# Performance work log

Hardware: AMD Instinct MI355X
Metric: run time of the kernel (lower is better)

Reference implementation:

```python
import jax, jax.numpy as jnp
import numpy as np
from functools import partial

EPS = 1e-6

def rmsnorm(x, w):
    rms = jnp.sqrt(jnp.mean(x * x, axis=-1, keepdims=True) + EPS)
    return x * w / rms

def causal_dwconv(x, w):
    # x: [B, T, D], w: [D, 1, k] depthwise kernel (torch Conv1d layout)
    D = x.shape[-1]
    k = w.shape[-1]
    xt = jnp.transpose(x, (0, 2, 1))  # [B, D, T]
    out = jax.lax.conv_general_dilated(
        xt, w, window_strides=(1,), padding=[(k - 1, 0)],
        dimension_numbers=("NCH", "OIH", "NCH"), feature_group_count=D)
    return jnp.transpose(out, (0, 2, 1))  # [B, T, D]

def setup_inputs() -> dict:
    key = jax.random.key(0)
    B, T, D, F, S = 2, 4096, 1024, 4096, 4096
    ks = jax.random.split(key, 20)
    s = 0.02
    return {
        "x": jax.random.normal(ks[0], (B, T, D), jnp.float32),
        "h_prev": jnp.zeros((B, D), jnp.float32),
        "norm1_w": jnp.ones((D,), jnp.float32),
        "conv3_w": jax.random.normal(ks[1], (D, 1, 3), jnp.float32) * s,
        "conv7_w": jax.random.normal(ks[2], (D, 1, 7), jnp.float32) * s,
        "conv15_w": jax.random.normal(ks[3], (D, 1, 15), jnp.float32) * s,
        "mix_w": jax.random.normal(ks[4], (D, D), jnp.float32) * s,
        "norm2_w": jnp.ones((D,), jnp.float32),
        "Wz_w": jax.random.normal(ks[5], (D, D), jnp.float32) * s,
        "Wz_b": jnp.zeros((D,), jnp.float32),
        "Wh_w": jax.random.normal(ks[6], (D, D), jnp.float32) * s,
        "Wh_b": jnp.zeros((D,), jnp.float32),
        "norm3_w": jnp.ones((D,), jnp.float32),
        "slot_keys": jax.random.normal(ks[7], (S, D), jnp.float32) * s,
        "slot_values": jax.random.normal(ks[8], (S, D), jnp.float32) * s,
        "projq_w": jax.random.normal(ks[9], (D, D), jnp.float32) * s,
        "projout_w": jax.random.normal(ks[10], (D, D), jnp.float32) * s,
        "norm4_w": jnp.ones((D,), jnp.float32),
        "gate_w": jax.random.normal(ks[11], (F, D), jnp.float32) * s,
        "up_w": jax.random.normal(ks[12], (F, D), jnp.float32) * s,
        "down_w": jax.random.normal(ks[13], (D, F), jnp.float32) * s,
    }

def resonance_forward(x, h_prev, norm1_w, conv3_w, conv7_w, conv15_w, mix_w,
                      norm2_w, Wz_w, Wz_b, Wh_w, Wh_b, norm3_w, slot_keys,
                      slot_values, projq_w, projout_w, norm4_w, gate_w, up_w, down_w):
    B, T, D = x.shape
    top_k = 2
    # 1. multi-scale causal conv block
    xn = rmsnorm(x, norm1_w)
    conv = causal_dwconv(xn, conv3_w) + causal_dwconv(xn, conv7_w) + causal_dwconv(xn, conv15_w)
    x = x + conv @ mix_w.T
    # 2. MinGRU: precompute gates, then linear recurrence via scan
    xn = rmsnorm(x, norm2_w)
    z = jax.nn.sigmoid(xn @ Wz_w.T + Wz_b)        # [B, T, D]
    h_tilde = xn @ Wh_w.T + Wh_b                  # [B, T, D]
    def step(h, zh):
        zt, ht = zh
        h = (1.0 - zt) * h + zt * ht
        return h, h
    h_last, hs = jax.lax.scan(step, h_prev,
                              (jnp.swapaxes(z, 0, 1), jnp.swapaxes(h_tilde, 0, 1)))
    x = x + jnp.swapaxes(hs, 0, 1)
    # 3. slot memory with top-k routing
    xn = rmsnorm(x, norm3_w)
    q = xn @ projq_w.T
    scores = (q @ slot_keys.T) / jnp.sqrt(jnp.asarray(D, x.dtype))  # [B, T, S]
    topk_vals, topk_ids = jax.lax.top_k(scores, top_k)              # [B, T, k]
    attn = jax.nn.softmax(topk_vals, axis=-1)
    gathered = slot_values[topk_ids]                                # [B, T, k, D]
    retrieved = jnp.einsum("btk,btkd->btd", attn, gathered)
    x = x + retrieved @ projout_w.T
    # 4. SwiGLU FFN
    xn = rmsnorm(x, norm4_w)
    ff = (jax.nn.silu(xn @ gate_w.T) * (xn @ up_w.T)) @ down_w.T
    x = x + ff
    return x, h_last

def reference(x, h_prev, norm1_w, conv3_w, conv7_w, conv15_w, mix_w, norm2_w,
              Wz_w, Wz_b, Wh_w, Wh_b, norm3_w, slot_keys, slot_values,
              projq_w, projout_w, norm4_w, gate_w, up_w, down_w):
    return resonance_forward(x, h_prev, norm1_w, conv3_w, conv7_w, conv15_w,
                             mix_w, norm2_w, Wz_w, Wz_b, Wh_w, Wh_b, norm3_w,
                             slot_keys, slot_values, projq_w, projout_w,
                             norm4_w, gate_w, up_w, down_w)
```

## Files before the change

### kernel.cpp

```cpp
#include <hip/hip_runtime.h>
#include <hip/hip_bf16.h>
#include <cstdint>

#define BB   2
#define TT   4096
#define DD   1024
#define FF   4096
#define SS   4096
#define MTOK (BB * TT)
#define NCHUNK 32
#define TCHUNK 128

typedef __bf16 bf16x8 __attribute__((ext_vector_type(8)));
typedef float  f32x4  __attribute__((ext_vector_type(4)));
typedef __attribute__((address_space(3))) char lds_char;
typedef __attribute__((address_space(1))) char g_char;

struct CvtArgs {
  const float* src[9];
  __hip_bfloat16* dst[9];
  int off4[10];
};

__global__ __launch_bounds__(256) void cvt_all_kernel(CvtArgs a) {
  int g = blockIdx.x * 256 + threadIdx.x;
  if (g >= a.off4[9]) return;
  int s = 0;
  while (g >= a.off4[s + 1]) s++;
  int i = g - a.off4[s];
  float4 v = ((const float4*)a.src[s])[i];
  union { ushort4 u; __hip_bfloat16 h[4]; } p;
  p.h[0] = __float2bfloat16(v.x);
  p.h[1] = __float2bfloat16(v.y);
  p.h[2] = __float2bfloat16(v.z);
  p.h[3] = __float2bfloat16(v.w);
  ((ushort4*)a.dst[s])[i] = p.u;
}

__global__ void wcomb_kernel(const float* __restrict__ w3, const float* __restrict__ w7,
                             const float* __restrict__ w15, float* __restrict__ wc) {
  int d = blockIdx.x * 256 + threadIdx.x;
  if (d >= DD) return;
  for (int j = 0; j < 16; j++) {
    float v = 0.f;
    if (j < 15) {
      v = w15[d * 15 + (14 - j)];
      if (j < 7) v += w7[d * 7 + (6 - j)];
      if (j < 3) v += w3[d * 3 + (2 - j)];
    }
    wc[d * 16 + j] = v;
  }
}

__global__ __launch_bounds__(256) void rms_kernel(const float* __restrict__ x,
                                                  const float* __restrict__ w,
                                                  __hip_bfloat16* __restrict__ ob) {
  const int row = blockIdx.x;
  const int tid = threadIdx.x;
  float4 v = ((const float4*)(x + (size_t)row * DD))[tid];
  float ss = v.x * v.x + v.y * v.y + v.z * v.z + v.w * v.w;
  for (int off = 32; off > 0; off >>= 1) ss += __shfl_down(ss, off, 64);
  __shared__ float wsum[4];
  if ((tid & 63) == 0) wsum[tid >> 6] = ss;
  __syncthreads();
  float tot = wsum[0] + wsum[1] + wsum[2] + wsum[3];
  float rinv = 1.0f / sqrtf(tot * (1.0f / DD) + 1e-6f);
  float4 wg = ((const float4*)w)[tid];
  union { ushort4 u; __hip_bfloat16 h[4]; } p;
  p.h[0] = __float2bfloat16(v.x * wg.x * rinv);
  p.h[1] = __float2bfloat16(v.y * wg.y * rinv);
  p.h[2] = __float2bfloat16(v.z * wg.z * rinv);
  p.h[3] = __float2bfloat16(v.w * wg.w * rinv);
  ((ushort4*)ob)[(size_t)row * 256 + tid] = p.u;
}

__global__ __launch_bounds__(256) void conv_kernel(const __hip_bfloat16* __restrict__ xn,
                                                   const float* __restrict__ wc,
                                                   __hip_bfloat16* __restrict__ outp) {
  __shared__ float xt[78][64];
  __shared__ float wt[64][15];
  const int b = blockIdx.z, t0 = blockIdx.x * 64, d0 = blockIdx.y * 64;
  const int tid = threadIdx.x;
  const int dl = tid & 63;
  for (int idx = tid; idx < 64 * 15; idx += 256) {
    int d = idx / 15, j = idx % 15;
    wt[d][j] = wc[(d0 + d) * 16 + j];
  }
  for (int r = tid >> 6; r < 78; r += 4) {
    int t = t0 - 14 + r;
    xt[r][dl] = (t >= 0) ? __bfloat162float(xn[((size_t)b * TT + t) * DD + d0 + dl]) : 0.f;
  }
  __syncthreads();
  for (int tl = tid >> 6; tl < 64; tl += 4) {
    float acc = 0.f;
#pragma unroll
    for (int j = 0; j < 15; j++) acc += wt[dl][j] * xt[tl + 14 - j][dl];
    outp[((size_t)b * TT + t0 + tl) * DD + d0 + dl] = __float2bfloat16(acc);
  }
}

template <int EPI>
__global__ __launch_bounds__(256, 2) void gemm_bt(
    const __hip_bfloat16* __restrict__ A, const __hip_bfloat16* __restrict__ Bm,
    const int M, const int N, const int K,
    const float* __restrict__ resid, float* __restrict__ outf,
    __hip_bfloat16* __restrict__ outb,
    const float* __restrict__ bias0, const float* __restrict__ bias1,
    const __hip_bfloat16* __restrict__ mulin) {
  __shared__ __align__(16) __hip_bfloat16 As[128 * 32];
  __shared__ __align__(16) __hip_bfloat16 Bs[128 * 32];
  const int tid = threadIdx.x;
  const int lane = tid & 63;
  const int wave = tid >> 6;
  const int fm = lane & 15, fq = lane >> 4;

  const int nT = gridDim.x;
  const int lin = blockIdx.y * nT + blockIdx.x;
  const int xcd = lin & 7;
  const int idx_ = lin >> 3;
  const int mq = idx_ / nT;
  const int tileM = (xcd * (gridDim.y >> 3) + mq) * 128;
  const int tileN = (idx_ - mq * nT) * 128;

  const int wm = (wave & 1) * 64, wn = (wave >> 1) * 64;

  f32x4 acc[4][4] = {};

  const int srow = tid >> 2;
  const int scol = (tid & 3) * 8;
  const __hip_bfloat16* gA = A + (size_t)(tileM + srow) * K + scol;
  const __hip_bfloat16* gB = Bm + (size_t)(tileN + srow) * K + scol;
  lds_char* ldsA = (lds_char*)(&As[0]);
  lds_char* ldsB = (lds_char*)(&Bs[0]);
  const int wbyte = wave * 1024;

  for (int k0 = 0; k0 < K; k0 += 32) {
    __syncthreads();
    __builtin_amdgcn_global_load_lds((g_char*)(void*)(gA + k0),                  ldsA + wbyte,        16, 0, 0);
    __builtin_amdgcn_global_load_lds((g_char*)(void*)(gA + k0 + (size_t)64 * K), ldsA + wbyte + 4096, 16, 0, 0);
    __builtin_amdgcn_global_load_lds((g_char*)(void*)(gB + k0),                  ldsB + wbyte,        16, 0, 0);
    __builtin_amdgcn_global_load_lds((g_char*)(void*)(gB + k0 + (size_t)64 * K), ldsB + wbyte + 4096, 16, 0, 0);
    __syncthreads();
    bf16x8 af[4], bfr[4];
#pragma unroll
    for (int i = 0; i < 4; i++) {
      af[i]  = *(const bf16x8*)(As + (wm + i * 16 + fm) * 32 + fq * 8);
      bfr[i] = *(const bf16x8*)(Bs + (wn + i * 16 + fm) * 32 + fq * 8);
    }
#pragma unroll
    for (int i = 0; i < 4; i++)
#pragma unroll
      for (int j = 0; j < 4; j++)
        acc[i][j] = __builtin_amdgcn_mfma_f32_16x16x32_bf16(af[i], bfr[j], acc[i][j], 0, 0, 0);
  }

#pragma unroll
  for (int i = 0; i < 4; i++) {
#pragma unroll
    for (int j = 0; j < 4; j++) {
      const int c = tileN + wn + j * 16 + fm;
#pragma unroll
      for (int r = 0; r < 4; r++) {
        const int rw = tileM + wm + i * 16 + fq * 4 + r;
        const size_t idx = (size_t)rw * N + c;
        float v = acc[i][j][r];
        if constexpr (EPI == 0) {
          outf[idx] = resid[idx] + v;
        } else if constexpr (EPI == 1) {
          v += (c < DD) ? bias0[c] : bias1[c - DD];
          if (c < DD) v = 1.f / (1.f + __expf(-v));
          outb[idx] = __float2bfloat16(v);
        } else if constexpr (EPI == 2) {
          outb[idx] = __float2bfloat16(v);
        } else if constexpr (EPI == 4) {
          outb[idx] = __float2bfloat16(v / (1.f + __expf(-v)));
        } else {
          outb[idx] = __float2bfloat16(v * __bfloat162float(mulin[idx]));
        }
      }
    }
  }
}

__global__ __launch_bounds__(256) void scan_pass1(const __hip_bfloat16* __restrict__ zht,
                                                  float* __restrict__ cA,
                                                  float* __restrict__ cB) {
  const int b = blockIdx.z, c = blockIdx.y;
  const int d = blockIdx.x * 256 + threadIdx.x;
  const __hip_bfloat16* base = zht + (size_t)b * TT * 2048;
  float A = 1.f, Bc = 0.f;
  const int t0 = c * TCHUNK;
  for (int t = t0; t < t0 + TCHUNK; t++) {
    const __hip_bfloat16* rowp = base + (size_t)t * 2048;
    float z = __bfloat162float(rowp[d]);
    float h = __bfloat162float(rowp[DD + d]);
    float om = 1.f - z;
    A *= om;
    Bc = om * Bc + z * h;
  }
  size_t idx = ((size_t)b * NCHUNK + c) * DD + d;
  cA[idx] = A;
  cB[idx] = Bc;
}

__global__ __launch_bounds__(256) void scan_pass2(const float* __restrict__ hp,
                                                  const float* __restrict__ cA,
                                                  const float* __restrict__ cB,
                                                  float* __restrict__ hstart,
                                                  float* __restrict__ hlast) {
  const int b = blockIdx.y;
  const int d = blockIdx.x * 256 + threadIdx.x;
  float h = hp[b * DD + d];
  for (int c = 0; c < NCHUNK; c++) {
    size_t idx = ((size_t)b * NCHUNK + c) * DD + d;
    hstart[idx] = h;
    h = cA[idx] * h + cB[idx];
  }
  hlast[b * DD + d] = h;
}

__global__ __launch_bounds__(256) void scan_pass3(const __hip_bfloat16* __restrict__ zht,
                                                  const float* __restrict__ hstart,
                                                  float* __restrict__ x) {
  const int b = blockIdx.z, c = blockIdx.y;
  const int d = blockIdx.x * 256 + threadIdx.x;
  const __hip_bfloat16* base = zht + (size_t)b * TT * 2048;
  float h = hstart[((size_t)b * NCHUNK + c) * DD + d];
  const int t0 = c * TCHUNK;
  for (int t = t0; t < t0 + TCHUNK; t++) {
    const __hip_bfloat16* rowp = base + (size_t)t * 2048;
    float z = __bfloat162float(rowp[d]);
    float ht = __bfloat162float(rowp[DD + d]);
    h = (1.f - z) * h + z * ht;
    x[((size_t)b * TT + t) * DD + d] += h;
  }
}

__global__ __launch_bounds__(256) void topk_kernel(const __hip_bfloat16* __restrict__ scores,
                                                   const float* __restrict__ sv,
                                                   __hip_bfloat16* __restrict__ ret) {
  const int row = blockIdx.x;
  const int tid = threadIdx.x;
  const __hip_bfloat16* sr = scores + (size_t)row * SS;
  float v0 = -3.4e38f, v1 = -3.4e38f;
  int i0 = 0x7fffffff, i1 = 0x7fffffff;
#pragma unroll
  for (int it = 0; it < 2; it++) {
    int j0 = (it * 256 + tid) * 8;
    bf16x8 v8 = *(const bf16x8*)(sr + j0);
#pragma unroll
    for (int k = 0; k < 8; k++) {
      float v = (float)v8[k];
      int j = j0 + k;
      if (v > v0) { v1 = v0; i1 = i0; v0 = v; i0 = j; }
      else if (v > v1) { v1 = v; i1 = j; }
    }
  }
#define TKMERGE(w0, j0, w1, j1)                                              \
  {                                                                          \
    if (w0 > v0 || (w0 == v0 && j0 < i0)) {                                  \
      float t0v = v0; int t0i = i0; v0 = w0; i0 = j0;                        \
      if (t0v > w1 || (t0v == w1 && t0i < j1)) { v1 = t0v; i1 = t0i; }       \
      else { v1 = w1; i1 = j1; }                                             \
    } else {                                                                 \
      if (w0 > v1 || (w0 == v1 && j0 < i1)) { v1 = w0; i1 = j0; }            \
    }                                                                        \
  }
  for (int off = 32; off > 0; off >>= 1) {
    float w0 = __shfl_down(v0, off, 64), w1 = __shfl_down(v1, off, 64);
    int   j0 = __shfl_down(i0, off, 64), j1 = __shfl_down(i1, off, 64);
    TKMERGE(w0, j0, w1, j1);
  }
  __shared__ float wv0[4], wv1[4];
  __shared__ int   wi0[4], wi1[4];
  __shared__ float sattn[2];
  __shared__ int   sidx[2];
  if ((tid & 63) == 0) { int w = tid >> 6; wv0[w] = v0; wv1[w] = v1; wi0[w] = i0; wi1[w] = i1; }
  __syncthreads();
  if (tid == 0) {
    v0 = wv0[0]; i0 = wi0[0]; v1 = wv1[0]; i1 = wi1[0];
    for (int w = 1; w < 4; w++) { TKMERGE(wv0[w], wi0[w], wv1[w], wi1[w]); }
    float s0 = v0 * (1.f / 32.f), s1 = v1 * (1.f / 32.f);
    float e = __expf(s1 - s0);
    float denom = 1.f + e;
    sattn[0] = 1.f / denom;
    sattn[1] = e / denom;
    sidx[0] = i0; sidx[1] = i1;
  }
  __syncthreads();
  float a0 = sattn[0], a1 = sattn[1];
  const float4* r0 = (const float4*)(sv + (size_t)sidx[0] * DD);
  const float4* r1 = (const float4*)(sv + (size_t)sidx[1] * DD);
  float4 u = r0[tid], w4 = r1[tid];
  union { ushort4 u; __hip_bfloat16 h[4]; } p;
  p.h[0] = __float2bfloat16(a0 * u.x + a1 * w4.x);
  p.h[1] = __float2bfloat16(a0 * u.y + a1 * w4.y);
  p.h[2] = __float2bfloat16(a0 * u.z + a1 * w4.z);
  p.h[3] = __float2bfloat16(a0 * u.w + a1 * w4.w);
  ((ushort4*)(ret + (size_t)row * DD))[tid] = p.u;
#undef TKMERGE
}

extern "C" void kernel_launch(void* const* d_in, const int* in_sizes, int n_in,
                              void* d_out, int out_size, void* d_ws, size_t ws_size,
                              hipStream_t stream) {
  (void)in_sizes; (void)n_in; (void)out_size; (void)ws_size;
  const float* x_in   = (const float*)d_in[0];
  const float* h_prev = (const float*)d_in[1];
  const float* n1w    = (const float*)d_in[2];
  const float* w3     = (const float*)d_in[3];
  const float* w7     = (const float*)d_in[4];
  const float* w15    = (const float*)d_in[5];
  const float* mixw   = (const float*)d_in[6];
  const float* n2w    = (const float*)d_in[7];
  const float* wzw    = (const float*)d_in[8];
  const float* wzb    = (const float*)d_in[9];
  const float* whw    = (const float*)d_in[10];
  const float* whb    = (const float*)d_in[11];
  const float* n3w    = (const float*)d_in[12];
  const float* slotk  = (const float*)d_in[13];
  const float* slotv  = (const float*)d_in[14];
  const float* pqw    = (const float*)d_in[15];
  const float* pow_   = (const float*)d_in[16];
  const float* n4w    = (const float*)d_in[17];
  const float* gatew  = (const float*)d_in[18];
  const float* upw    = (const float*)d_in[19];
  const float* downw  = (const float*)d_in[20];
  float* out = (float*)d_out;

  char* ws = (char*)d_ws;
  size_t o = 0;
  auto alloc = [&](size_t bytes) {
    size_t r = o;
    o += (bytes + 255) & ~(size_t)255;
    return r;
  };
  __hip_bfloat16* wmix = (__hip_bfloat16*)(ws + alloc((size_t)DD * DD * 2));
  __hip_bfloat16* wzht = (__hip_bfloat16*)(ws + alloc((size_t)2 * DD * DD * 2));
  __hip_bfloat16* wpq  = (__hip_bfloat16*)(ws + alloc((size_t)DD * DD * 2));
  __hip_bfloat16* wsk  = (__hip_bfloat16*)(ws + alloc((size_t)SS * DD * 2));
  __hip_bfloat16* wpo  = (__hip_bfloat16*)(ws + alloc((size_t)DD * DD * 2));
  __hip_bfloat16* wg   = (__hip_bfloat16*)(ws + alloc((size_t)FF * DD * 2));
  __hip_bfloat16* wu   = (__hip_bfloat16*)(ws + alloc((size_t)FF * DD * 2));
  __hip_bfloat16* wd   = (__hip_bfloat16*)(ws + alloc((size_t)DD * FF * 2));
  float* wcomb = (float*)(ws + alloc((size_t)DD * 16 * 4));
  float* xws   = (float*)(ws + alloc((size_t)MTOK * DD * 4));
  __hip_bfloat16* xnb  = (__hip_bfloat16*)(ws + alloc((size_t)MTOK * DD * 2));
  __hip_bfloat16* qb   = (__hip_bfloat16*)(ws + alloc((size_t)MTOK * DD * 2));
  __hip_bfloat16* retr = (__hip_bfloat16*)(ws + alloc((size_t)MTOK * DD * 2));
  float* scanA  = (float*)(ws + alloc((size_t)BB * NCHUNK * DD * 4));
  float* scanB  = (float*)(ws + alloc((size_t)BB * NCHUNK * DD * 4));
  float* hstart = (float*)(ws + alloc((size_t)BB * NCHUNK * DD * 4));
  char* big = ws + alloc((size_t)MTOK * FF * 4);
  __hip_bfloat16* xn1b  = (__hip_bfloat16*)big;
  __hip_bfloat16* convb = (__hip_bfloat16*)(big + (size_t)MTOK * DD * 2);
  __hip_bfloat16* zhtb  = (__hip_bfloat16*)big;
  __hip_bfloat16* scoresb = (__hip_bfloat16*)big;
  __hip_bfloat16* sg    = (__hip_bfloat16*)big;
  __hip_bfloat16* ffin  = (__hip_bfloat16*)(big + (size_t)MTOK * FF * 2);

  {
    CvtArgs a;
    const float* srcs[9] = {mixw, wzw, whw, pqw, slotk, pow_, gatew, upw, downw};
    __hip_bfloat16* dsts[9] = {wmix, wzht, wzht + (size_t)DD * DD, wpq, wsk, wpo, wg, wu, wd};
    int n4s[9] = {DD * DD / 4, DD * DD / 4, DD * DD / 4, DD * DD / 4, SS * DD / 4,
                  DD * DD / 4, FF * DD / 4, FF * DD / 4, DD * FF / 4};
    int acc_ = 0;
    for (int i = 0; i < 9; i++) { a.src[i] = srcs[i]; a.dst[i] = dsts[i]; a.off4[i] = acc_; acc_ += n4s[i]; }
    a.off4[9] = acc_;
    cvt_all_kernel<<<(acc_ + 255) / 256, 256, 0, stream>>>(a);
  }
  wcomb_kernel<<<DD / 256, 256, 0, stream>>>(w3, w7, w15, wcomb);

  rms_kernel<<<MTOK, 256, 0, stream>>>(x_in, n1w, xn1b);
  conv_kernel<<<dim3(TT / 64, DD / 64, BB), 256, 0, stream>>>(xn1b, wcomb, convb);
  gemm_bt<0><<<dim3(DD / 128, MTOK / 128), 256, 0, stream>>>(
      convb, wmix, MTOK, DD, DD, x_in, xws, nullptr, nullptr, nullptr, nullptr);

  rms_kernel<<<MTOK, 256, 0, stream>>>(xws, n2w, xnb);
  gemm_bt<1><<<dim3(2048 / 128, MTOK / 128), 256, 0, stream>>>(
      xnb, wzht, MTOK, 2048, DD, nullptr, nullptr, zhtb, wzb, whb, nullptr);
  scan_pass1<<<dim3(DD / 256, NCHUNK, BB), 256, 0, stream>>>(zhtb, scanA, scanB);
  scan_pass2<<<dim3(DD / 256, BB), 256, 0, stream>>>(h_prev, scanA, scanB, hstart,
                                                     out + (size_t)MTOK * DD);
  scan_pass3<<<dim3(DD / 256, NCHUNK, BB), 256, 0, stream>>>(zhtb, hstart, xws);

  rms_kernel<<<MTOK, 256, 0, stream>>>(xws, n3w, xnb);
  gemm_bt<2><<<dim3(DD / 128, MTOK / 128), 256, 0, stream>>>(
      xnb, wpq, MTOK, DD, DD, nullptr, nullptr, qb, nullptr, nullptr, nullptr);
  gemm_bt<2><<<dim3(SS / 128, MTOK / 128), 256, 0, stream>>>(
      qb, wsk, MTOK, SS, DD, nullptr, nullptr, scoresb, nullptr, nullptr, nullptr);
  topk_kernel<<<MTOK, 256, 0, stream>>>(scoresb, slotv, retr);
  gemm_bt<0><<<dim3(DD / 128, MTOK / 128), 256, 0, stream>>>(
      retr, wpo, MTOK, DD, DD, xws, xws, nullptr, nullptr, nullptr, nullptr);

  rms_kernel<<<MTOK, 256, 0, stream>>>(xws, n4w, xnb);
  gemm_bt<4><<<dim3(FF / 128, MTOK / 128), 256, 0, stream>>>(
      xnb, wg, MTOK, FF, DD, nullptr, nullptr, sg, nullptr, nullptr, nullptr);
  gemm_bt<5><<<dim3(FF / 128, MTOK / 128), 256, 0, stream>>>(
      xnb, wu, MTOK, FF, DD, nullptr, nullptr, ffin, nullptr, nullptr, sg);
  gemm_bt<0><<<dim3(DD / 128, MTOK / 128), 256, 0, stream>>>(
      ffin, wd, MTOK, DD, FF, xws, out, nullptr, nullptr, nullptr, nullptr);
}
```

Measured before the change: 799.7 us.

## Fuse gate/up GEMMs, split-K the down projection, use 64-row tiles for small GEMMs

The gate and up weights are interleaved in 16-row groups during bf16 conversion, so one GEMM produces both and applies SiLU(g)*u in its epilogue. This removes the separate intermediate activation buffer and its write and read. The down projection is split along K into two partial fp32 buffers, and a new reduce kernel sums them with the residual, to raise block count. The D×D GEMMs switch to a 64-row tile variant for more blocks and occupancy. In exchange, split-K adds fp32 partial traffic and an extra launch.

```diff
diff --git a/kernel.cpp b/kernel.cpp
--- a/kernel.cpp
+++ b/kernel.cpp
@@ -20,6 +20,7 @@
   const float* src[9];
   __hip_bfloat16* dst[9];
   int off4[10];
+  int mode[9];
 };
 
 __global__ __launch_bounds__(256) void cvt_all_kernel(CvtArgs a) {
@@ -34,7 +35,14 @@
   p.h[1] = __float2bfloat16(v.y);
   p.h[2] = __float2bfloat16(v.z);
   p.h[3] = __float2bfloat16(v.w);
-  ((ushort4*)a.dst[s])[i] = p.u;
+  int di = i;
+  int m = a.mode[s];
+  if (m) {
+    int r = i >> 8, c = i & 255;
+    int dr = ((r >> 4) << 5) + (r & 15) + ((m == 2) ? 16 : 0);
+    di = (dr << 8) + c;
+  }
+  ((ushort4*)a.dst[s])[di] = p.u;
 }
 
 __global__ void wcomb_kernel(const float* __restrict__ w3, const float* __restrict__ w7,
@@ -99,14 +107,12 @@
   }
 }
 
-template <int EPI>
+template <int EPI, int KSPLIT = 1>
 __global__ __launch_bounds__(256, 2) void gemm_bt(
     const __hip_bfloat16* __restrict__ A, const __hip_bfloat16* __restrict__ Bm,
     const int M, const int N, const int K,
-    const float* __restrict__ resid, float* __restrict__ outf,
-    __hip_bfloat16* __restrict__ outb,
-    const float* __restrict__ bias0, const float* __restrict__ bias1,
-    const __hip_bfloat16* __restrict__ mulin) {
+    float* __restrict__ outf, __hip_bfloat16* __restrict__ outb,
+    const float* __restrict__ bias0, const float* __restrict__ bias1) {
   __shared__ __align__(16) __hip_bfloat16 As[128 * 32];
   __shared__ __align__(16) __hip_bfloat16 Bs[128 * 32];
   const int tid = threadIdx.x;
@@ -134,7 +140,9 @@
   lds_char* ldsB = (lds_char*)(&Bs[0]);
   const int wbyte = wave * 1024;
 
-  for (int k0 = 0; k0 < K; k0 += 32) {
+  const int kPer = K / KSPLIT;
+  const int kBeg = (KSPLIT > 1) ? blockIdx.z * kPer : 0;
+  for (int k0 = kBeg; k0 < kBeg + kPer; k0 += 32) {
     __syncthreads();
     __builtin_amdgcn_global_load_lds((g_char*)(void*)(gA + k0),                  ldsA + wbyte,        16, 0, 0);
     __builtin_amdgcn_global_load_lds((g_char*)(void*)(gA + k0 + (size_t)64 * K), ldsA + wbyte + 4096, 16, 0, 0);
@@ -154,8 +162,103 @@
         acc[i][j] = __builtin_amdgcn_mfma_f32_16x16x32_bf16(af[i], bfr[j], acc[i][j], 0, 0, 0);
   }
 
-#pragma unroll
-  for (int i = 0; i < 4; i++) {
+  if constexpr (EPI == 7) {
+#pragma unroll
+    for (int i = 0; i < 4; i++) {
+#pragma unroll
+      for (int j = 0; j < 4; j += 2) {
+        const int ffcol = (((tileN + wn + j * 16) >> 5) << 4) + fm;
+#pragma unroll
+        for (int r = 0; r < 4; r++) {
+          const int rw = tileM + wm + i * 16 + fq * 4 + r;
+          float g = acc[i][j][r];
+          float u = acc[i][j + 1][r];
+          float v = g / (1.f + __expf(-g)) * u;
+          outb[(size_t)rw * FF + ffcol] = __float2bfloat16(v);
+        }
+      }
+    }
+  } else {
+#pragma unroll
+    for (int i = 0; i < 4; i++) {
+#pragma unroll
+      for (int j = 0; j < 4; j++) {
+        const int c = tileN + wn + j * 16 + fm;
+#pragma unroll
+        for (int r = 0; r < 4; r++) {
+          const int rw = tileM + wm + i * 16 + fq * 4 + r;
+          const size_t idx = (size_t)rw * N + c;
+          float v = acc[i][j][r];
+          if constexpr (EPI == 1) {
+            v += (c < DD) ? bias0[c] : bias1[c - DD];
+            if (c < DD) v = 1.f / (1.f + __expf(-v));
+            outb[idx] = __float2bfloat16(v);
+          } else if constexpr (EPI == 2) {
+            outb[idx] = __float2bfloat16(v);
+          } else if constexpr (EPI == 6) {
+            outf[(size_t)blockIdx.z * M * N + idx] = v;
+          }
+        }
+      }
+    }
+  }
+}
+
+template <int EPI>
+__global__ __launch_bounds__(256, 4) void gemm_bt64(
+    const __hip_bfloat16* __restrict__ A, const __hip_bfloat16* __restrict__ Bm,
+    const int M, const int N, const int K,
+    const float* __restrict__ resid, float* __restrict__ outf,
+    __hip_bfloat16* __restrict__ outb) {
+  __shared__ __align__(16) __hip_bfloat16 As[64 * 32];
+  __shared__ __align__(16) __hip_bfloat16 Bs[128 * 32];
+  const int tid = threadIdx.x;
+  const int lane = tid & 63;
+  const int wave = tid >> 6;
+  const int fm = lane & 15, fq = lane >> 4;
+
+  const int nT = gridDim.x;
+  const int lin = blockIdx.y * nT + blockIdx.x;
+  const int xcd = lin & 7;
+  const int idx_ = lin >> 3;
+  const int mq = idx_ / nT;
+  const int tileM = (xcd * (gridDim.y >> 3) + mq) * 64;
+  const int tileN = (idx_ - mq * nT) * 128;
+
+  const int wm = (wave & 1) * 32, wn = (wave >> 1) * 64;
+
+  f32x4 acc[2][4] = {};
+
+  const int srow = tid >> 2;
+  const int scol = (tid & 3) * 8;
+  const __hip_bfloat16* gA = A + (size_t)(tileM + srow) * K + scol;
+  const __hip_bfloat16* gB = Bm + (size_t)(tileN + srow) * K + scol;
+  lds_char* ldsA = (lds_char*)(&As[0]);
+  lds_char* ldsB = (lds_char*)(&Bs[0]);
+  const int wbyte = wave * 1024;
+
+  for (int k0 = 0; k0 < K; k0 += 32) {
+    __syncthreads();
+    __builtin_amdgcn_global_load_lds((g_char*)(void*)(gA + k0),                  ldsA + wbyte,        16, 0, 0);
+    __builtin_amdgcn_global_load_lds((g_char*)(void*)(gB + k0),                  ldsB + wbyte,        16, 0, 0);
+    __builtin_amdgcn_global_load_lds((g_char*)(void*)(gB + k0 + (size_t)64 * K), ldsB + wbyte + 4096, 16, 0, 0);
+    __syncthreads();
+    bf16x8 af[2], bfr[4];
+#pragma unroll
+    for (int i = 0; i < 2; i++)
+      af[i]  = *(const bf16x8*)(As + (wm + i * 16 + fm) * 32 + fq * 8);
+#pragma unroll
+    for (int j = 0; j < 4; j++)
+      bfr[j] = *(const bf16x8*)(Bs + (wn + j * 16 + fm) * 32 + fq * 8);
+#pragma unroll
+    for (int i = 0; i < 2; i++)
+#pragma unroll
+      for (int j = 0; j < 4; j++)
+        acc[i][j] = __builtin_amdgcn_mfma_f32_16x16x32_bf16(af[i], bfr[j], acc[i][j], 0, 0, 0);
+  }
+
+#pragma unroll
+  for (int i = 0; i < 2; i++) {
 #pragma unroll
     for (int j = 0; j < 4; j++) {
       const int c = tileN + wn + j * 16 + fm;
@@ -166,20 +269,25 @@
         float v = acc[i][j][r];
         if constexpr (EPI == 0) {
           outf[idx] = resid[idx] + v;
-        } else if constexpr (EPI == 1) {
-          v += (c < DD) ? bias0[c] : bias1[c - DD];
-          if (c < DD) v = 1.f / (1.f + __expf(-v));
+        } else {
           outb[idx] = __float2bfloat16(v);
-        } else if constexpr (EPI == 2) {
-          outb[idx] = __float2bfloat16(v);
-        } else if constexpr (EPI == 4) {
-          outb[idx] = __float2bfloat16(v / (1.f + __expf(-v)));
-        } else {
-          outb[idx] = __float2bfloat16(v * __bfloat162float(mulin[idx]));
         }
       }
     }
   }
+}
+
+__global__ __launch_bounds__(256) void reduce_down(const float* __restrict__ P,
+                                                   const float* __restrict__ resid,
+                                                   float* __restrict__ out) {
+  size_t i = (size_t)blockIdx.x * 256 + threadIdx.x;
+  float4 a = ((const float4*)P)[i];
+  float4 b = ((const float4*)(P + (size_t)MTOK * DD))[i];
+  float4 rr = ((const float4*)resid)[i];
+  float4 o;
+  o.x = rr.x + a.x + b.x; o.y = rr.y + a.y + b.y;
+  o.z = rr.z + a.z + b.z; o.w = rr.w + a.w + b.w;
+  ((float4*)out)[i] = o;
 }
 
 __global__ __launch_bounds__(256) void scan_pass1(const __hip_bfloat16* __restrict__ zht,
@@ -340,8 +448,7 @@
   __hip_bfloat16* wpq  = (__hip_bfloat16*)(ws + alloc((size_t)DD * DD * 2));
   __hip_bfloat16* wsk  = (__hip_bfloat16*)(ws + alloc((size_t)SS * DD * 2));
   __hip_bfloat16* wpo  = (__hip_bfloat16*)(ws + alloc((size_t)DD * DD * 2));
-  __hip_bfloat16* wg   = (__hip_bfloat16*)(ws + alloc((size_t)FF * DD * 2));
-  __hip_bfloat16* wu   = (__hip_bfloat16*)(ws + alloc((size_t)FF * DD * 2));
+  __hip_bfloat16* wfu  = (__hip_bfloat16*)(ws + alloc((size_t)2 * FF * DD * 2));
   __hip_bfloat16* wd   = (__hip_bfloat16*)(ws + alloc((size_t)DD * FF * 2));
   float* wcomb = (float*)(ws + alloc((size_t)DD * 16 * 4));
   float* xws   = (float*)(ws + alloc((size_t)MTOK * DD * 4));
@@ -356,17 +463,21 @@
   __hip_bfloat16* convb = (__hip_bfloat16*)(big + (size_t)MTOK * DD * 2);
   __hip_bfloat16* zhtb  = (__hip_bfloat16*)big;
   __hip_bfloat16* scoresb = (__hip_bfloat16*)big;
-  __hip_bfloat16* sg    = (__hip_bfloat16*)big;
-  __hip_bfloat16* ffin  = (__hip_bfloat16*)(big + (size_t)MTOK * FF * 2);
+  __hip_bfloat16* ffin  = (__hip_bfloat16*)big;
+  float* Pbuf           = (float*)(big + (size_t)MTOK * FF * 2);
 
   {
     CvtArgs a;
     const float* srcs[9] = {mixw, wzw, whw, pqw, slotk, pow_, gatew, upw, downw};
-    __hip_bfloat16* dsts[9] = {wmix, wzht, wzht + (size_t)DD * DD, wpq, wsk, wpo, wg, wu, wd};
+    __hip_bfloat16* dsts[9] = {wmix, wzht, wzht + (size_t)DD * DD, wpq, wsk, wpo, wfu, wfu, wd};
     int n4s[9] = {DD * DD / 4, DD * DD / 4, DD * DD / 4, DD * DD / 4, SS * DD / 4,
                   DD * DD / 4, FF * DD / 4, FF * DD / 4, DD * FF / 4};
+    int modes[9] = {0, 0, 0, 0, 0, 0, 1, 2, 0};
     int acc_ = 0;
-    for (int i = 0; i < 9; i++) { a.src[i] = srcs[i]; a.dst[i] = dsts[i]; a.off4[i] = acc_; acc_ += n4s[i]; }
+    for (int i = 0; i < 9; i++) {
+      a.src[i] = srcs[i]; a.dst[i] = dsts[i]; a.off4[i] = acc_; a.mode[i] = modes[i];
+      acc_ += n4s[i];
+    }
     a.off4[9] = acc_;
     cvt_all_kernel<<<(acc_ + 255) / 256, 256, 0, stream>>>(a);
   }
@@ -374,31 +485,30 @@
 
   rms_kernel<<<MTOK, 256, 0, stream>>>(x_in, n1w, xn1b);
   conv_kernel<<<dim3(TT / 64, DD / 64, BB), 256, 0, stream>>>(xn1b, wcomb, convb);
-  gemm_bt<0><<<dim3(DD / 128, MTOK / 128), 256, 0, stream>>>(
-      convb, wmix, MTOK, DD, DD, x_in, xws, nullptr, nullptr, nullptr, nullptr);
+  gemm_bt64<0><<<dim3(DD / 128, MTOK / 64), 256, 0, stream>>>(
+      convb, wmix, MTOK, DD, DD, x_in, xws, nullptr);
 
   rms_kernel<<<MTOK, 256, 0, stream>>>(xws, n2w, xnb);
   gemm_bt<1><<<dim3(2048 / 128, MTOK / 128), 256, 0, stream>>>(
-      xnb, wzht, MTOK, 2048, DD, nullptr, nullptr, zhtb, wzb, whb, nullptr);
+      xnb, wzht, MTOK, 2048, DD, nullptr, zhtb, wzb, whb);
   scan_pass1<<<dim3(DD / 256, NCHUNK, BB), 256, 0, stream>>>(zhtb, scanA, scanB);
   scan_pass2<<<dim3(DD / 256, BB), 256, 0, stream>>>(h_prev, scanA, scanB, hstart,
                                                      out + (size_t)MTOK * DD);
   scan_pass3<<<dim3(DD / 256, NCHUNK, BB), 256, 0, stream>>>(zhtb, hstart, xws);
 
   rms_kernel<<<MTOK, 256, 0, stream>>>(xws, n3w, xnb);
-  gemm_bt<2><<<dim3(DD / 128, MTOK / 128), 256, 0, stream>>>(
-      xnb, wpq, MTOK, DD, DD, nullptr, nullptr, qb, nullptr, nullptr, nullptr);
+  gemm_bt64<2><<<dim3(DD / 128, MTOK / 64), 256, 0, stream>>>(
+      xnb, wpq, MTOK, DD, DD, nullptr, nullptr, qb);
   gemm_bt<2><<<dim3(SS / 128, MTOK / 128), 256, 0, stream>>>(
-      qb, wsk, MTOK, SS, DD, nullptr, nullptr, scoresb, nullptr, nullptr, nullptr);
+      qb, wsk, MTOK, SS, DD, nullptr, scoresb, nullptr, nullptr);
   topk_kernel<<<MTOK, 256, 0, stream>>>(scoresb, slotv, retr);
-  gemm_bt<0><<<dim3(DD / 128, MTOK / 128), 256, 0, stream>>>(
-      retr, wpo, MTOK, DD, DD, xws, xws, nullptr, nullptr, nullptr, nullptr);
+  gemm_bt64<0><<<dim3(DD / 128, MTOK / 64), 256, 0, stream>>>(
+      retr, wpo, MTOK, DD, DD, xws, xws, nullptr);
 
   rms_kernel<<<MTOK, 256, 0, stream>>>(xws, n4w, xnb);
-  gemm_bt<4><<<dim3(FF / 128, MTOK / 128), 256, 0, stream>>>(
-      xnb, wg, MTOK, FF, DD, nullptr, nullptr, sg, nullptr, nullptr, nullptr);
-  gemm_bt<5><<<dim3(FF / 128, MTOK / 128), 256, 0, stream>>>(
-      xnb, wu, MTOK, FF, DD, nullptr, nullptr, ffin, nullptr, nullptr, sg);
-  gemm_bt<0><<<dim3(DD / 128, MTOK / 128), 256, 0, stream>>>(
-      ffin, wd, MTOK, DD, FF, xws, out, nullptr, nullptr, nullptr, nullptr);
-}
+  gemm_bt<7><<<dim3(2 * FF / 128, MTOK / 128), 256, 0, stream>>>(
+      xnb, wfu, MTOK, 2 * FF, DD, nullptr, ffin, nullptr, nullptr);
+  gemm_bt<6, 2><<<dim3(DD / 128, MTOK / 128, 2), 256, 0, stream>>>(
+      ffin, wd, MTOK, DD, FF, Pbuf, nullptr, nullptr, nullptr);
+  reduce_down<<<MTOK * DD / 1024, 256, 0, stream>>>(Pbuf, xws, out);
+}
```

Result: no change. 791.3 us (-1.1%).
